# Kernel tuning notes

Hardware: AMD Instinct MI355X
Metric: run time of the kernel (lower is better)

## Reference

```python
import jax, jax.numpy as jnp
import numpy as np

B, S, D, H = 2, 2048, 512, 8
DK = D // H


def setup_inputs() -> dict:
    key = jax.random.key(0)
    ks = jax.random.split(key, 7)
    scale = 1.0 / np.sqrt(D)
    return {
        "query": jax.random.normal(ks[0], (B, S, D), dtype=jnp.float32),
        "key": jax.random.normal(ks[1], (B, S, D), dtype=jnp.float32),
        "value": jax.random.normal(ks[2], (B, S, D), dtype=jnp.float32),
        "w_q": jax.random.normal(ks[3], (D, D), dtype=jnp.float32) * scale,
        "w_k": jax.random.normal(ks[4], (D, D), dtype=jnp.float32) * scale,
        "w_v": jax.random.normal(ks[5], (D, D), dtype=jnp.float32) * scale,
        "w_o": jax.random.normal(ks[6], (D, D), dtype=jnp.float32) * scale,
    }


def reference(query, key, value, w_q, w_k, w_v, w_o):
    # Linear projections (torch nn.Linear: x @ W.T), split into heads -> [b, h, s, dk]
    def proj(x, w):
        return (x @ w.T).reshape(B, -1, H, DK).transpose(0, 2, 1, 3)

    q = proj(query, w_q)
    k = proj(key, w_k)
    v = proj(value, w_v)

    # scaled dot-product attention (unfused, materializes [b,h,s,s] scores)
    scores = jnp.einsum("bhqd,bhkd->bhqk", q, k) / np.sqrt(DK)
    p_attn = jax.nn.softmax(scores, axis=-1)
    out = jnp.einsum("bhqk,bhkd->bhqd", p_attn, v)  # [b,h,s,dk]

    # merge heads and final projection
    out = out.transpose(0, 2, 1, 3).reshape(B, -1, D)
    out = out @ w_o.T
    return (out, p_attn)
```

## Files before the change

kernel.cpp:

```cpp
#include <hip/hip_runtime.h>
#include <hip/hip_bf16.h>
#include <cstdint>
#include <cstddef>

#define BB 2
#define SS 2048
#define DD 512
#define HH 8
#define DKK 64

typedef __attribute__((ext_vector_type(8))) short bf16x8;
typedef __attribute__((ext_vector_type(4))) float f32x4;

__device__ __forceinline__ unsigned short f2bf(float f) {
    union { float f; unsigned u; } v; v.f = f;
    unsigned u = v.u;
    return (unsigned short)((u + 0x7fffu + ((u >> 16) & 1u)) >> 16);
}
__device__ __forceinline__ unsigned pack2(float a, float b) {
    return (unsigned)f2bf(a) | ((unsigned)f2bf(b) << 16);
}

__global__ __launch_bounds__(256) void k_proj_qkv(
    const float* __restrict__ qin, const float* __restrict__ kin, const float* __restrict__ vin,
    const float* __restrict__ wq,  const float* __restrict__ wk,  const float* __restrict__ wv,
    unsigned short* __restrict__ Qw, unsigned short* __restrict__ Kw, unsigned short* __restrict__ Vt)
{
    __shared__ unsigned short smem[5120];
    unsigned short* Al = smem;
    unsigned short* Bl = smem + 2560;

    const int z = blockIdx.z;
    const float* X = (z == 0) ? qin : (z == 1) ? kin : vin;
    const float* W = (z == 0) ? wq  : (z == 1) ? wk  : wv;

    const int bm = blockIdx.x, bn = blockIdx.y;
    const int tid = threadIdx.x;
    const int w = tid >> 6, lane = tid & 63, quad = lane >> 4, l15 = lane & 15;
    const int sr = tid >> 2, sc = (tid & 3) * 8;

    f32x4 acc[4];
    #pragma unroll
    for (int i = 0; i < 4; ++i) acc[i] = (f32x4){0.f, 0.f, 0.f, 0.f};

    const float* ap = X + (size_t)(bm * 64 + sr) * DD + sc;
    const float* bp = W + (size_t)(bn * 64 + sr) * DD + sc;

    for (int k0 = 0; k0 < DD; k0 += 32) {
        float4 a0 = *(const float4*)(ap + k0);
        float4 a1 = *(const float4*)(ap + k0 + 4);
        float4 b0 = *(const float4*)(bp + k0);
        float4 b1 = *(const float4*)(bp + k0 + 4);
        uint4 av = make_uint4(pack2(a0.x,a0.y), pack2(a0.z,a0.w), pack2(a1.x,a1.y), pack2(a1.z,a1.w));
        uint4 bv = make_uint4(pack2(b0.x,b0.y), pack2(b0.z,b0.w), pack2(b1.x,b1.y), pack2(b1.z,b1.w));
        *(uint4*)&Al[sr * 40 + sc] = av;
        *(uint4*)&Bl[sr * 40 + sc] = bv;
        __syncthreads();
        bf16x8 a = *(const bf16x8*)&Al[(w * 16 + l15) * 40 + quad * 8];
        #pragma unroll
        for (int nt = 0; nt < 4; ++nt) {
            bf16x8 b = *(const bf16x8*)&Bl[(nt * 16 + l15) * 40 + quad * 8];
            acc[nt] = __builtin_amdgcn_mfma_f32_16x16x32_bf16(a, b, acc[nt], 0, 0, 0);
        }
        __syncthreads();
    }

    if (z < 2) {
        unsigned short* dst = z ? Kw : Qw;
        #pragma unroll
        for (int nt = 0; nt < 4; ++nt) {
            int n = bn * 64 + nt * 16 + l15;
            int h = n >> 6, dk = n & 63;
            #pragma unroll
            for (int rg = 0; rg < 4; ++rg) {
                int m = bm * 64 + w * 16 + quad * 4 + rg;
                int b = m >> 11, s = m & (SS - 1);
                dst[(((size_t)(b * HH + h) * SS + s) << 6) + dk] = f2bf(acc[nt][rg]);
            }
        }
    } else {
        unsigned short* T = smem;
        #pragma unroll
        for (int nt = 0; nt < 4; ++nt)
            #pragma unroll
            for (int rg = 0; rg < 4; ++rg)
                T[(w * 16 + quad * 4 + rg) * 72 + nt * 16 + l15] = f2bf(acc[nt][rg]);
        __syncthreads();
        int n = tid >> 2, s0 = (tid & 3) * 16;
        int ng = bn * 64 + n, h = ng >> 6, dk = ng & 63;
        int mg = bm * 64 + s0, b = mg >> 11, s = mg & (SS - 1);
        unsigned vals[8];
        #pragma unroll
        for (int i = 0; i < 8; ++i)
            vals[i] = (unsigned)T[(s0 + 2*i) * 72 + n] | ((unsigned)T[(s0 + 2*i + 1) * 72 + n] << 16);
        unsigned short* dp = Vt + ((size_t)(b * HH + h) * DKK + dk) * SS + s;
        ((uint4*)dp)[0] = make_uint4(vals[0], vals[1], vals[2], vals[3]);
        ((uint4*)dp)[1] = make_uint4(vals[4], vals[5], vals[6], vals[7]);
    }
}

__global__ __launch_bounds__(256) void k_attn(
    const unsigned short* __restrict__ Qw, const unsigned short* __restrict__ Kw,
    const unsigned short* __restrict__ Vt, unsigned short* __restrict__ AO,
    float* __restrict__ P)
{
    __shared__ unsigned short Pl[4][16][72];
    const int qt = blockIdx.x, bh = blockIdx.y;
    const int tid = threadIdx.x, w = tid >> 6, lane = tid & 63, quad = lane >> 4, l15 = lane & 15;

    const unsigned short* Qb = Qw + ((size_t)bh * SS + qt * 64 + w * 16) * DKK;
    const unsigned short* Kb = Kw + (size_t)bh * SS * DKK;
    const unsigned short* Vb = Vt + (size_t)bh * DKK * SS;

    bf16x8 qa0 = *(const bf16x8*)&Qb[l15 * DKK + quad * 8];
    bf16x8 qa1 = *(const bf16x8*)&Qb[l15 * DKK + 32 + quad * 8];

    f32x4 oacc[4];
    #pragma unroll
    for (int i = 0; i < 4; ++i) oacc[i] = (f32x4){0.f, 0.f, 0.f, 0.f};
    float lsum[4] = {0.f, 0.f, 0.f, 0.f};

    for (int kt = 0; kt < SS / 64; ++kt) {
        const unsigned short* Kt = Kb + (size_t)kt * 64 * DKK;
        f32x4 sa[4];
        #pragma unroll
        for (int i = 0; i < 4; ++i) sa[i] = (f32x4){0.f, 0.f, 0.f, 0.f};
        #pragma unroll
        for (int jt = 0; jt < 4; ++jt) {
            bf16x8 b0 = *(const bf16x8*)&Kt[(jt * 16 + l15) * DKK + quad * 8];
            bf16x8 b1 = *(const bf16x8*)&Kt[(jt * 16 + l15) * DKK + 32 + quad * 8];
            sa[jt] = __builtin_amdgcn_mfma_f32_16x16x32_bf16(qa0, b0, sa[jt], 0, 0, 0);
            sa[jt] = __builtin_amdgcn_mfma_f32_16x16x32_bf16(qa1, b1, sa[jt], 0, 0, 0);
        }
        float ev[4][4];
        #pragma unroll
        for (int jt = 0; jt < 4; ++jt)
            #pragma unroll
            for (int rg = 0; rg < 4; ++rg)
                ev[jt][rg] = __expf(sa[jt][rg] * 0.125f);
        #pragma unroll
        for (int rg = 0; rg < 4; ++rg) {
            float v = ev[0][rg] + ev[1][rg] + ev[2][rg] + ev[3][rg];
            v += __shfl_xor(v, 1);
            v += __shfl_xor(v, 2);
            v += __shfl_xor(v, 4);
            v += __shfl_xor(v, 8);
            lsum[rg] += v;
        }
        #pragma unroll
        for (int jt = 0; jt < 4; ++jt)
            #pragma unroll
            for (int rg = 0; rg < 4; ++rg)
                Pl[w][quad * 4 + rg][jt * 16 + l15] = f2bf(ev[jt][rg]);
        __syncthreads();
        bf16x8 pa0 = *(const bf16x8*)&Pl[w][l15][quad * 8];
        bf16x8 pa1 = *(const bf16x8*)&Pl[w][l15][32 + quad * 8];
        #pragma unroll
        for (int dt = 0; dt < 4; ++dt) {
            const unsigned short* Vp = Vb + (size_t)(dt * 16 + l15) * SS + kt * 64;
            bf16x8 v0 = *(const bf16x8*)&Vp[quad * 8];
            bf16x8 v1 = *(const bf16x8*)&Vp[32 + quad * 8];
            oacc[dt] = __builtin_amdgcn_mfma_f32_16x16x32_bf16(pa0, v0, oacc[dt], 0, 0, 0);
            oacc[dt] = __builtin_amdgcn_mfma_f32_16x16x32_bf16(pa1, v1, oacc[dt], 0, 0, 0);
        }
        __syncthreads();
    }

    float linv[4];
    #pragma unroll
    for (int rg = 0; rg < 4; ++rg) linv[rg] = 1.0f / lsum[rg];

    const int b = bh >> 3, h = bh & 7;
    const int srow = qt * 64 + w * 16 + quad * 4;
    #pragma unroll
    for (int dt = 0; dt < 4; ++dt)
        #pragma unroll
        for (int rg = 0; rg < 4; ++rg)
            AO[((size_t)(b * SS + srow + rg) << 9) + h * 64 + dt * 16 + l15] =
                f2bf(oacc[dt][rg] * linv[rg]);

    float* Pb = P + (((size_t)bh * SS + qt * 64 + w * 16 + quad * 4) << 11);
    for (int kt = 0; kt < SS / 64; ++kt) {
        const unsigned short* Kt = Kb + (size_t)kt * 64 * DKK;
        #pragma unroll
        for (int jt = 0; jt < 4; ++jt) {
            bf16x8 b0 = *(const bf16x8*)&Kt[(jt * 16 + l15) * DKK + quad * 8];
            bf16x8 b1 = *(const bf16x8*)&Kt[(jt * 16 + l15) * DKK + 32 + quad * 8];
            f32x4 sa = (f32x4){0.f, 0.f, 0.f, 0.f};
            sa = __builtin_amdgcn_mfma_f32_16x16x32_bf16(qa0, b0, sa, 0, 0, 0);
            sa = __builtin_amdgcn_mfma_f32_16x16x32_bf16(qa1, b1, sa, 0, 0, 0);
            #pragma unroll
            for (int rg = 0; rg < 4; ++rg)
                Pb[((size_t)rg << 11) + kt * 64 + jt * 16 + l15] =
                    __expf(sa[rg] * 0.125f) * linv[rg];
        }
    }
}

__global__ __launch_bounds__(256) void k_outproj(
    const unsigned short* __restrict__ AO, const float* __restrict__ Wo, float* __restrict__ Out)
{
    __shared__ unsigned short Al[64 * 40];
    __shared__ unsigned short Bl[64 * 40];
    const int bm = blockIdx.x, bn = blockIdx.y;
    const int tid = threadIdx.x, w = tid >> 6, lane = tid & 63, quad = lane >> 4, l15 = lane & 15;
    const int sr = tid >> 2, sc = (tid & 3) * 8;

    f32x4 acc[4];
    #pragma unroll
    for (int i = 0; i < 4; ++i) acc[i] = (f32x4){0.f, 0.f, 0.f, 0.f};

    const unsigned short* ap = AO + (size_t)(bm * 64 + sr) * DD + sc;
    const float* bp = Wo + (size_t)(bn * 64 + sr) * DD + sc;

    for (int k0 = 0; k0 < DD; k0 += 32) {
        uint4 av = *(const uint4*)(ap + k0);
        float4 b0 = *(const float4*)(bp + k0);
        float4 b1 = *(const float4*)(bp + k0 + 4);
        uint4 bv = make_uint4(pack2(b0.x,b0.y), pack2(b0.z,b0.w), pack2(b1.x,b1.y), pack2(b1.z,b1.w));
        *(uint4*)&Al[sr * 40 + sc] = av;
        *(uint4*)&Bl[sr * 40 + sc] = bv;
        __syncthreads();
        bf16x8 a = *(const bf16x8*)&Al[(w * 16 + l15) * 40 + quad * 8];
        #pragma unroll
        for (int nt = 0; nt < 4; ++nt) {
            bf16x8 b = *(const bf16x8*)&Bl[(nt * 16 + l15) * 40 + quad * 8];
            acc[nt] = __builtin_amdgcn_mfma_f32_16x16x32_bf16(a, b, acc[nt], 0, 0, 0);
        }
        __syncthreads();
    }
    #pragma unroll
    for (int nt = 0; nt < 4; ++nt)
        #pragma unroll
        for (int rg = 0; rg < 4; ++rg)
            Out[(size_t)(bm * 64 + w * 16 + quad * 4 + rg) * DD + bn * 64 + nt * 16 + l15] =
                acc[nt][rg];
}

extern "C" void kernel_launch(void* const* d_in, const int* in_sizes, int n_in,
                              void* d_out, int out_size, void* d_ws, size_t ws_size,
                              hipStream_t stream) {
    const float* q  = (const float*)d_in[0];
    const float* k  = (const float*)d_in[1];
    const float* v  = (const float*)d_in[2];
    const float* wq = (const float*)d_in[3];
    const float* wk = (const float*)d_in[4];
    const float* wv = (const float*)d_in[5];
    const float* wo = (const float*)d_in[6];

    const size_t elems = (size_t)BB * HH * SS * DKK;
    unsigned short* Qw = (unsigned short*)d_ws;
    unsigned short* Kw = Qw + elems;
    unsigned short* Vt = Kw + elems;
    unsigned short* AO = Vt + elems;

    float* out = (float*)d_out;
    float* P   = out + (size_t)BB * SS * DD;

    k_proj_qkv<<<dim3(64, 8, 3), 256, 0, stream>>>(q, k, v, wq, wk, wv, Qw, Kw, Vt);
    k_attn   <<<dim3(SS / 64, BB * HH), 256, 0, stream>>>(Qw, Kw, Vt, AO, P);
    k_outproj<<<dim3(64, 8), 256, 0, stream>>>(AO, wo, out);
}
```

Before: 486.0 us.

## Pre-convert inputs to bf16, use async LDS loads, split P-write into separate kernel

Adds a conversion kernel that casts all fp32 inputs and weights to bf16 into the P output buffer, which is used as scratch, and replaces the projection GEMMs with a templated kernel that uses global_load_lds with XOR-swizzled LDS and a K-step of 64. The 1/sqrt(dk) scale is folded into Q. The attention loop double-buffers the per-warp P tile, which removes the block barriers. The probability write moves to a separate kernel gridded over key splits using stored row inverse sums. This trades extra launches and a bf16 conversion pass for better GEMM loads and more parallelism in the large P write.

```diff
diff --git a/kernel.cpp b/kernel.cpp
--- a/kernel.cpp
+++ b/kernel.cpp
@@ -21,52 +21,80 @@
     return (unsigned)f2bf(a) | ((unsigned)f2bf(b) << 16);
 }
 
-__global__ __launch_bounds__(256) void k_proj_qkv(
-    const float* __restrict__ qin, const float* __restrict__ kin, const float* __restrict__ vin,
-    const float* __restrict__ wq,  const float* __restrict__ wk,  const float* __restrict__ wv,
-    unsigned short* __restrict__ Qw, unsigned short* __restrict__ Kw, unsigned short* __restrict__ Vt)
-{
-    __shared__ unsigned short smem[5120];
-    unsigned short* Al = smem;
-    unsigned short* Bl = smem + 2560;
-
-    const int z = blockIdx.z;
-    const float* X = (z == 0) ? qin : (z == 1) ? kin : vin;
-    const float* W = (z == 0) ? wq  : (z == 1) ? wk  : wv;
-
+typedef const __attribute__((address_space(1))) unsigned int* gp_t;
+typedef __attribute__((address_space(3))) unsigned int* lp_t;
+__device__ __forceinline__ void gload_lds16(const void* g, void* l) {
+    __builtin_amdgcn_global_load_lds((gp_t)g, (lp_t)l, 16, 0, 0);
+}
+
+__global__ __launch_bounds__(256) void k_cvt(
+    const float* __restrict__ q, const float* __restrict__ k, const float* __restrict__ v,
+    const float* __restrict__ wq, const float* __restrict__ wk, const float* __restrict__ wv,
+    const float* __restrict__ wo, unsigned short* __restrict__ dst)
+{
+    const size_t NX = (size_t)BB * SS * DD;
+    const size_t NW = (size_t)DD * DD;
+    const int y = blockIdx.y;
+    const float* src; unsigned short* d; int n;
+    switch (y) {
+        case 0: src = q;  d = dst;                 n = (int)NX; break;
+        case 1: src = k;  d = dst + NX;            n = (int)NX; break;
+        case 2: src = v;  d = dst + 2 * NX;        n = (int)NX; break;
+        case 3: src = wq; d = dst + 3 * NX;        n = (int)NW; break;
+        case 4: src = wk; d = dst + 3 * NX + NW;   n = (int)NW; break;
+        case 5: src = wv; d = dst + 3 * NX + 2*NW; n = (int)NW; break;
+        default: src = wo; d = dst + 3 * NX + 3*NW; n = (int)NW; break;
+    }
+    int idx = (blockIdx.x * 256 + threadIdx.x) * 8;
+    if (idx >= n) return;
+    float4 a = *(const float4*)(src + idx);
+    float4 b = *(const float4*)(src + idx + 4);
+    *(uint4*)(d + idx) = make_uint4(pack2(a.x,a.y), pack2(a.z,a.w), pack2(b.x,b.y), pack2(b.z,b.w));
+}
+
+template <int MODE>
+__global__ __launch_bounds__(256) void k_gemm64(
+    const unsigned short* __restrict__ A, const unsigned short* __restrict__ W,
+    unsigned short* __restrict__ dbf, float* __restrict__ df)
+{
+    __shared__ unsigned short smem[8192];
     const int bm = blockIdx.x, bn = blockIdx.y;
-    const int tid = threadIdx.x;
-    const int w = tid >> 6, lane = tid & 63, quad = lane >> 4, l15 = lane & 15;
-    const int sr = tid >> 2, sc = (tid & 3) * 8;
+    const int tid = threadIdx.x, w = tid >> 6, lane = tid & 63, quad = lane >> 4, l15 = lane & 15;
 
     f32x4 acc[4];
     #pragma unroll
     for (int i = 0; i < 4; ++i) acc[i] = (f32x4){0.f, 0.f, 0.f, 0.f};
 
-    const float* ap = X + (size_t)(bm * 64 + sr) * DD + sc;
-    const float* bp = W + (size_t)(bn * 64 + sr) * DD + sc;
-
-    for (int k0 = 0; k0 < DD; k0 += 32) {
-        float4 a0 = *(const float4*)(ap + k0);
-        float4 a1 = *(const float4*)(ap + k0 + 4);
-        float4 b0 = *(const float4*)(bp + k0);
-        float4 b1 = *(const float4*)(bp + k0 + 4);
-        uint4 av = make_uint4(pack2(a0.x,a0.y), pack2(a0.z,a0.w), pack2(a1.x,a1.y), pack2(a1.z,a1.w));
-        uint4 bv = make_uint4(pack2(b0.x,b0.y), pack2(b0.z,b0.w), pack2(b1.x,b1.y), pack2(b1.z,b1.w));
-        *(uint4*)&Al[sr * 40 + sc] = av;
-        *(uint4*)&Bl[sr * 40 + sc] = bv;
+    for (int k0 = 0; k0 < DD; k0 += 64) {
+        #pragma unroll
+        for (int r = 0; r < 2; ++r) {
+            int flat = r * 256 + tid;
+            int row = flat >> 3, c = flat & 7, cs = c ^ (row & 7);
+            gload_lds16(A + (size_t)(bm * 64 + row) * DD + k0 + cs * 8, &smem[flat * 8]);
+        }
+        #pragma unroll
+        for (int r = 0; r < 2; ++r) {
+            int flat = r * 256 + tid;
+            int row = flat >> 3, c = flat & 7, cs = c ^ (row & 7);
+            gload_lds16(W + (size_t)(bn * 64 + row) * DD + k0 + cs * 8, &smem[4096 + flat * 8]);
+        }
         __syncthreads();
-        bf16x8 a = *(const bf16x8*)&Al[(w * 16 + l15) * 40 + quad * 8];
+        int mrow = w * 16 + l15;
+        bf16x8 a0 = *(const bf16x8*)&smem[(mrow * 8 + (quad ^ (mrow & 7))) * 8];
+        bf16x8 a1 = *(const bf16x8*)&smem[(mrow * 8 + ((quad + 4) ^ (mrow & 7))) * 8];
         #pragma unroll
         for (int nt = 0; nt < 4; ++nt) {
-            bf16x8 b = *(const bf16x8*)&Bl[(nt * 16 + l15) * 40 + quad * 8];
-            acc[nt] = __builtin_amdgcn_mfma_f32_16x16x32_bf16(a, b, acc[nt], 0, 0, 0);
+            int nrow = nt * 16 + l15;
+            bf16x8 b0 = *(const bf16x8*)&smem[4096 + (nrow * 8 + (quad ^ (nrow & 7))) * 8];
+            bf16x8 b1 = *(const bf16x8*)&smem[4096 + (nrow * 8 + ((quad + 4) ^ (nrow & 7))) * 8];
+            acc[nt] = __builtin_amdgcn_mfma_f32_16x16x32_bf16(a0, b0, acc[nt], 0, 0, 0);
+            acc[nt] = __builtin_amdgcn_mfma_f32_16x16x32_bf16(a1, b1, acc[nt], 0, 0, 0);
         }
         __syncthreads();
     }
 
-    if (z < 2) {
-        unsigned short* dst = z ? Kw : Qw;
+    if (MODE == 0 || MODE == 1) {
+        const float sc = (MODE == 0) ? 0.125f : 1.0f;
         #pragma unroll
         for (int nt = 0; nt < 4; ++nt) {
             int n = bn * 64 + nt * 16 + l15;
@@ -75,10 +103,10 @@
             for (int rg = 0; rg < 4; ++rg) {
                 int m = bm * 64 + w * 16 + quad * 4 + rg;
                 int b = m >> 11, s = m & (SS - 1);
-                dst[(((size_t)(b * HH + h) * SS + s) << 6) + dk] = f2bf(acc[nt][rg]);
+                dbf[(((size_t)(b * HH + h) * SS + s) << 6) + dk] = f2bf(acc[nt][rg] * sc);
             }
         }
-    } else {
+    } else if (MODE == 2) {
         unsigned short* T = smem;
         #pragma unroll
         for (int nt = 0; nt < 4; ++nt)
@@ -93,18 +121,25 @@
         #pragma unroll
         for (int i = 0; i < 8; ++i)
             vals[i] = (unsigned)T[(s0 + 2*i) * 72 + n] | ((unsigned)T[(s0 + 2*i + 1) * 72 + n] << 16);
-        unsigned short* dp = Vt + ((size_t)(b * HH + h) * DKK + dk) * SS + s;
+        unsigned short* dp = dbf + ((size_t)(b * HH + h) * DKK + dk) * SS + s;
         ((uint4*)dp)[0] = make_uint4(vals[0], vals[1], vals[2], vals[3]);
         ((uint4*)dp)[1] = make_uint4(vals[4], vals[5], vals[6], vals[7]);
+    } else {
+        #pragma unroll
+        for (int nt = 0; nt < 4; ++nt)
+            #pragma unroll
+            for (int rg = 0; rg < 4; ++rg)
+                df[(size_t)(bm * 64 + w * 16 + quad * 4 + rg) * DD + bn * 64 + nt * 16 + l15] =
+                    acc[nt][rg];
     }
 }
 
 __global__ __launch_bounds__(256) void k_attn(
     const unsigned short* __restrict__ Qw, const unsigned short* __restrict__ Kw,
     const unsigned short* __restrict__ Vt, unsigned short* __restrict__ AO,
-    float* __restrict__ P)
-{
-    __shared__ unsigned short Pl[4][16][72];
+    float* __restrict__ Linv)
+{
+    __shared__ unsigned short Pl[2][4][16][68];
     const int qt = blockIdx.x, bh = blockIdx.y;
     const int tid = threadIdx.x, w = tid >> 6, lane = tid & 63, quad = lane >> 4, l15 = lane & 15;
 
@@ -120,7 +155,9 @@
     for (int i = 0; i < 4; ++i) oacc[i] = (f32x4){0.f, 0.f, 0.f, 0.f};
     float lsum[4] = {0.f, 0.f, 0.f, 0.f};
 
+    #pragma unroll 2
     for (int kt = 0; kt < SS / 64; ++kt) {
+        const int buf = kt & 1;
         const unsigned short* Kt = Kb + (size_t)kt * 64 * DKK;
         f32x4 sa[4];
         #pragma unroll
@@ -137,24 +174,23 @@
         for (int jt = 0; jt < 4; ++jt)
             #pragma unroll
             for (int rg = 0; rg < 4; ++rg)
-                ev[jt][rg] = __expf(sa[jt][rg] * 0.125f);
+                ev[jt][rg] = __expf(sa[jt][rg]);
         #pragma unroll
         for (int rg = 0; rg < 4; ++rg) {
-            float v = ev[0][rg] + ev[1][rg] + ev[2][rg] + ev[3][rg];
-            v += __shfl_xor(v, 1);
-            v += __shfl_xor(v, 2);
-            v += __shfl_xor(v, 4);
-            v += __shfl_xor(v, 8);
-            lsum[rg] += v;
+            float s = ev[0][rg] + ev[1][rg] + ev[2][rg] + ev[3][rg];
+            s += __shfl_xor(s, 1);
+            s += __shfl_xor(s, 2);
+            s += __shfl_xor(s, 4);
+            s += __shfl_xor(s, 8);
+            lsum[rg] += s;
         }
         #pragma unroll
         for (int jt = 0; jt < 4; ++jt)
             #pragma unroll
             for (int rg = 0; rg < 4; ++rg)
-                Pl[w][quad * 4 + rg][jt * 16 + l15] = f2bf(ev[jt][rg]);
-        __syncthreads();
-        bf16x8 pa0 = *(const bf16x8*)&Pl[w][l15][quad * 8];
-        bf16x8 pa1 = *(const bf16x8*)&Pl[w][l15][32 + quad * 8];
+                Pl[buf][w][quad * 4 + rg][jt * 16 + l15] = f2bf(ev[jt][rg]);
+        bf16x8 pa0 = *(const bf16x8*)&Pl[buf][w][l15][quad * 8];
+        bf16x8 pa1 = *(const bf16x8*)&Pl[buf][w][l15][32 + quad * 8];
         #pragma unroll
         for (int dt = 0; dt < 4; ++dt) {
             const unsigned short* Vp = Vb + (size_t)(dt * 16 + l15) * SS + kt * 64;
@@ -163,7 +199,6 @@
             oacc[dt] = __builtin_amdgcn_mfma_f32_16x16x32_bf16(pa0, v0, oacc[dt], 0, 0, 0);
             oacc[dt] = __builtin_amdgcn_mfma_f32_16x16x32_bf16(pa1, v1, oacc[dt], 0, 0, 0);
         }
-        __syncthreads();
     }
 
     float linv[4];
@@ -179,8 +214,33 @@
             AO[((size_t)(b * SS + srow + rg) << 9) + h * 64 + dt * 16 + l15] =
                 f2bf(oacc[dt][rg] * linv[rg]);
 
-    float* Pb = P + (((size_t)bh * SS + qt * 64 + w * 16 + quad * 4) << 11);
-    for (int kt = 0; kt < SS / 64; ++kt) {
+    if (l15 == 0) {
+        #pragma unroll
+        for (int rg = 0; rg < 4; ++rg)
+            Linv[(size_t)bh * SS + srow + rg] = linv[rg];
+    }
+}
+
+__global__ __launch_bounds__(256) void k_pwrite(
+    const unsigned short* __restrict__ Qw, const unsigned short* __restrict__ Kw,
+    const float* __restrict__ Linv, float* __restrict__ P)
+{
+    const int qt = blockIdx.x, bh = blockIdx.y, ks = blockIdx.z;
+    const int tid = threadIdx.x, w = tid >> 6, lane = tid & 63, quad = lane >> 4, l15 = lane & 15;
+
+    const unsigned short* Qb = Qw + ((size_t)bh * SS + qt * 64 + w * 16) * DKK;
+    bf16x8 qa0 = *(const bf16x8*)&Qb[l15 * DKK + quad * 8];
+    bf16x8 qa1 = *(const bf16x8*)&Qb[l15 * DKK + 32 + quad * 8];
+
+    float linv[4];
+    #pragma unroll
+    for (int rg = 0; rg < 4; ++rg)
+        linv[rg] = Linv[(size_t)bh * SS + qt * 64 + w * 16 + quad * 4 + rg];
+
+    const unsigned short* Kb = Kw + (size_t)bh * SS * DKK + (size_t)ks * 512 * DKK;
+    float* Pb = P + (((size_t)bh * SS + qt * 64 + w * 16 + quad * 4) << 11) + ks * 512;
+
+    for (int kt = 0; kt < 8; ++kt) {
         const unsigned short* Kt = Kb + (size_t)kt * 64 * DKK;
         #pragma unroll
         for (int jt = 0; jt < 4; ++jt) {
@@ -191,50 +251,9 @@
             sa = __builtin_amdgcn_mfma_f32_16x16x32_bf16(qa1, b1, sa, 0, 0, 0);
             #pragma unroll
             for (int rg = 0; rg < 4; ++rg)
-                Pb[((size_t)rg << 11) + kt * 64 + jt * 16 + l15] =
-                    __expf(sa[rg] * 0.125f) * linv[rg];
-        }
-    }
-}
-
-__global__ __launch_bounds__(256) void k_outproj(
-    const unsigned short* __restrict__ AO, const float* __restrict__ Wo, float* __restrict__ Out)
-{
-    __shared__ unsigned short Al[64 * 40];
-    __shared__ unsigned short Bl[64 * 40];
-    const int bm = blockIdx.x, bn = blockIdx.y;
-    const int tid = threadIdx.x, w = tid >> 6, lane = tid & 63, quad = lane >> 4, l15 = lane & 15;
-    const int sr = tid >> 2, sc = (tid & 3) * 8;
-
-    f32x4 acc[4];
-    #pragma unroll
-    for (int i = 0; i < 4; ++i) acc[i] = (f32x4){0.f, 0.f, 0.f, 0.f};
-
-    const unsigned short* ap = AO + (size_t)(bm * 64 + sr) * DD + sc;
-    const float* bp = Wo + (size_t)(bn * 64 + sr) * DD + sc;
-
-    for (int k0 = 0; k0 < DD; k0 += 32) {
-        uint4 av = *(const uint4*)(ap + k0);
-        float4 b0 = *(const float4*)(bp + k0);
-        float4 b1 = *(const float4*)(bp + k0 + 4);
-        uint4 bv = make_uint4(pack2(b0.x,b0.y), pack2(b0.z,b0.w), pack2(b1.x,b1.y), pack2(b1.z,b1.w));
-        *(uint4*)&Al[sr * 40 + sc] = av;
-        *(uint4*)&Bl[sr * 40 + sc] = bv;
-        __syncthreads();
-        bf16x8 a = *(const bf16x8*)&Al[(w * 16 + l15) * 40 + quad * 8];
-        #pragma unroll
-        for (int nt = 0; nt < 4; ++nt) {
-            bf16x8 b = *(const bf16x8*)&Bl[(nt * 16 + l15) * 40 + quad * 8];
-            acc[nt] = __builtin_amdgcn_mfma_f32_16x16x32_bf16(a, b, acc[nt], 0, 0, 0);
-        }
-        __syncthreads();
-    }
-    #pragma unroll
-    for (int nt = 0; nt < 4; ++nt)
-        #pragma unroll
-        for (int rg = 0; rg < 4; ++rg)
-            Out[(size_t)(bm * 64 + w * 16 + quad * 4 + rg) * DD + bn * 64 + nt * 16 + l15] =
-                acc[nt][rg];
+                Pb[((size_t)rg << 11) + kt * 64 + jt * 16 + l15] = __expf(sa[rg]) * linv[rg];
+        }
+    }
 }
 
 extern "C" void kernel_launch(void* const* d_in, const int* in_sizes, int n_in,
@@ -248,16 +267,31 @@
     const float* wv = (const float*)d_in[5];
     const float* wo = (const float*)d_in[6];
 
-    const size_t elems = (size_t)BB * HH * SS * DKK;
-    unsigned short* Qw = (unsigned short*)d_ws;
-    unsigned short* Kw = Qw + elems;
-    unsigned short* Vt = Kw + elems;
-    unsigned short* AO = Vt + elems;
-
     float* out = (float*)d_out;
     float* P   = out + (size_t)BB * SS * DD;
 
-    k_proj_qkv<<<dim3(64, 8, 3), 256, 0, stream>>>(q, k, v, wq, wk, wv, Qw, Kw, Vt);
-    k_attn   <<<dim3(SS / 64, BB * HH), 256, 0, stream>>>(Qw, Kw, Vt, AO, P);
-    k_outproj<<<dim3(64, 8), 256, 0, stream>>>(AO, wo, out);
-}
+    const size_t NX = (size_t)BB * SS * DD;
+    const size_t NW = (size_t)DD * DD;
+    unsigned short* scratch = (unsigned short*)P;
+    unsigned short* Xq = scratch;
+    unsigned short* Xk = scratch + NX;
+    unsigned short* Xv = scratch + 2 * NX;
+    unsigned short* Wq = scratch + 3 * NX;
+    unsigned short* Wk = Wq + NW;
+    unsigned short* Wv = Wk + NW;
+    unsigned short* Wo = Wv + NW;
+    unsigned short* AO = Wo + NW;
+
+    unsigned short* Qw = (unsigned short*)d_ws;
+    unsigned short* Kw = Qw + NX;
+    unsigned short* Vt = Kw + NX;
+    float* Linv = (float*)(Vt + NX);
+
+    k_cvt<<<dim3(1024, 7), 256, 0, stream>>>(q, k, v, wq, wk, wv, wo, scratch);
+    k_gemm64<0><<<dim3(64, 8), 256, 0, stream>>>(Xq, Wq, Qw, nullptr);
+    k_gemm64<1><<<dim3(64, 8), 256, 0, stream>>>(Xk, Wk, Kw, nullptr);
+    k_gemm64<2><<<dim3(64, 8), 256, 0, stream>>>(Xv, Wv, Vt, nullptr);
+    k_attn<<<dim3(SS / 64, BB * HH), 256, 0, stream>>>(Qw, Kw, Vt, AO, Linv);
+    k_gemm64<3><<<dim3(64, 8), 256, 0, stream>>>(AO, Wo, nullptr, out);
+    k_pwrite<<<dim3(SS / 64, BB * HH, 4), 256, 0, stream>>>(Qw, Kw, Linv, P);
+}
```

Measured after the change: 485.3 us. About the same (-0.1%).
